# Optimization experiments

Hardware: AMD Instinct MI355X
Metric: run time of the kernel (lower is better)

The kernel has to match this reference:

```python
import jax, jax.numpy as jnp
import numpy as np
from jax import lax

N, D, H = 4096, 768, 16384


def setup_inputs() -> dict:
    key = jax.random.key(0)
    k0, k1, k2, k3, k4, k5, k6 = jax.random.split(key, 7)
    bound_e = 1.0 / np.sqrt(D)   # kaiming_uniform(a=sqrt(5)) on (H, D) -> bound 1/sqrt(fan_in)
    bound_d = 1.0 / np.sqrt(H)   # nn.Linear default init, fan_in = H
    return {
        "vision_embeddings": jax.random.normal(k0, (N, D), dtype=jnp.float32),
        "text_embeddings": jax.random.normal(k1, (N, D), dtype=jnp.float32),
        "encoder": jax.random.uniform(k2, (H, D), jnp.float32, -bound_e, bound_e),
        "Wv": jax.random.uniform(k3, (D, H), jnp.float32, -bound_d, bound_d),
        "bv": jax.random.uniform(k4, (D,), jnp.float32, -bound_d, bound_d),
        "Wt": jax.random.uniform(k5, (D, H), jnp.float32, -bound_d, bound_d),
        "bt": jax.random.uniform(k6, (D,), jnp.float32, -bound_d, bound_d),
        "topk": 32,
    }


def _l2norm(x, axis):
    return x / jnp.maximum(jnp.linalg.norm(x, axis=axis, keepdims=True), 1e-12)


def _encode(emb, encoder, topk):
    # F.normalize rows, then cdist(p=2) between unit vectors: ||a-b|| = sqrt(2-2 a.b)
    w = _l2norm(encoder, axis=1)            # [H, D]
    e = _l2norm(emb, axis=1)                # [N, D]
    cos = jnp.einsum("nd,hd->nh", e, w)     # [N, H]
    dist = jnp.sqrt(jnp.maximum(2.0 - 2.0 * cos, 0.0))
    sim = 2.0 - dist                         # [N, H]
    # kthvalue(abs, k=H-topk) == (topk+1)-th largest; keep strictly-greater entries
    abs_f = jnp.abs(sim)
    thres = lax.top_k(abs_f, topk + 1)[0][:, -1]  # [N]
    mask = (abs_f > thres[:, None]).astype(sim.dtype)
    return sim * mask


def reference(vision_embeddings, text_embeddings, encoder, Wv, bv, Wt, bt, topk):
    latent_v = _encode(vision_embeddings, encoder, topk)          # [N, H]
    recon_v = jnp.einsum("nh,dh->nd", latent_v, Wv) + bv          # [N, D]
    latent_t = _encode(text_embeddings, encoder, topk)            # [N, H]
    recon_t = jnp.einsum("nh,dh->nd", latent_t, Wt) + bt          # [N, D]
    return (recon_v, recon_t, latent_v, latent_t)
```

## Files before the change

### kernel.cpp

```cpp
#include <hip/hip_runtime.h>
#include <math.h>


#define N_ROWS 4096
#define D_DIM  768
#define H_DIM  16384
#define M_TOT  8192
#define TOPK   32
#define MARGIN 1e-3f
#define SEL_CAP 40
#define AMB_CAP 64
#define CAP2   512

typedef __attribute__((ext_vector_type(8))) short short8;
typedef __attribute__((ext_vector_type(4))) float floatx4;

__device__ inline unsigned short bf16_rne(float f) {
    unsigned u = __float_as_uint(f);
    unsigned r = u + 0x7fffu + ((u >> 16) & 1u);
    return (unsigned short)(r >> 16);
}

__device__ inline void gload16(const unsigned short* g, unsigned short* l) {
    __builtin_amdgcn_global_load_lds(
        (const __attribute__((address_space(1))) void*)g,
        (__attribute__((address_space(3))) void*)l, 16, 0, 0);
}

__global__ void split_all_kernel(const float* __restrict__ embv,
                                 const float* __restrict__ embt,
                                 const float* __restrict__ enc,
                                 unsigned short* __restrict__ Ahi,
                                 unsigned short* __restrict__ Alo,
                                 unsigned short* __restrict__ Bh,
                                 float* __restrict__ invA,
                                 float* __restrict__ invB)
{
    int row = blockIdx.x;
    int tid = threadIdx.x;
    const float* src;
    unsigned short *hi, *lo;
    float* invp;
    if (row < N_ROWS) {
        src = embv + (size_t)row * D_DIM;
        hi = Ahi + (size_t)row * D_DIM; lo = Alo + (size_t)row * D_DIM;
        invp = invA + row;
    } else if (row < 2 * N_ROWS) {
        int r = row - N_ROWS;
        src = embt + (size_t)r * D_DIM;
        hi = Ahi + (size_t)row * D_DIM; lo = Alo + (size_t)row * D_DIM;
        invp = invA + row;
    } else {
        int r = row - 2 * N_ROWS;
        src = enc + (size_t)r * D_DIM;
        hi = Bh + (size_t)r * D_DIM; lo = nullptr;
        invp = invB + r;
    }
    __shared__ float red[4];
    const float4* s4 = reinterpret_cast<const float4*>(src);
    float4 v = make_float4(0.f, 0.f, 0.f, 0.f);
    float ss = 0.f;
    if (tid < 192) {
        v = s4[tid];
        ss = v.x * v.x + v.y * v.y + v.z * v.z + v.w * v.w;
    }
    #pragma unroll
    for (int o = 32; o > 0; o >>= 1) ss += __shfl_down(ss, o);
    int wave = tid >> 6, lane = tid & 63;
    if (lane == 0) red[wave] = ss;
    __syncthreads();
    if (tid == 0) {
        float tot = red[0] + red[1] + red[2];
        red[0] = 1.f / fmaxf(sqrtf(tot), 1e-12f);
    }
    __syncthreads();
    float inv = red[0];
    if (tid == 0) *invp = inv;
    if (tid < 192) {
        float x[4] = {v.x * inv, v.y * inv, v.z * inv, v.w * inv};
        unsigned short hh[4], ll[4];
        #pragma unroll
        for (int t = 0; t < 4; t++) {
            hh[t] = bf16_rne(x[t]);
            float hf = __uint_as_float((unsigned)hh[t] << 16);
            ll[t] = bf16_rne(x[t] - hf);
        }
        ushort4 h4; h4.x = hh[0]; h4.y = hh[1]; h4.z = hh[2]; h4.w = hh[3];
        *reinterpret_cast<ushort4*>(hi + tid * 4) = h4;
        if (lo) {
            ushort4 l4; l4.x = ll[0]; l4.y = ll[1]; l4.z = ll[2]; l4.w = ll[3];
            *reinterpret_cast<ushort4*>(lo + tid * 4) = l4;
        }
    }
}

#define GBK 32

__global__ __launch_bounds__(256, 4)
void gemm_mfma_kernel(const unsigned short* __restrict__ Ahi,
                      const unsigned short* __restrict__ Alo,
                      const unsigned short* __restrict__ Bh,
                      float* __restrict__ latent)
{
    __shared__ unsigned short sA[2][128 * GBK];
    __shared__ unsigned short sB[128 * GBK];

    int tid = threadIdx.x;
    int lane = tid & 63;
    int wave = tid >> 6;
    int wr = (wave >> 1) * 64;
    int wc = (wave & 1) * 64;
    int m = lane & 15;
    int q = lane >> 4;

    int row0 = blockIdx.y * 128;
    int col0 = blockIdx.x * 128;

    int p0 = tid, p1 = tid + 256;
    int r0 = ((p0 >> 5) << 3) | (p0 & 7), q0 = (p0 >> 3) & 3;
    int r1 = ((p1 >> 5) << 3) | (p1 & 7), q1 = (p1 >> 3) & 3;
    size_t aoff0 = (size_t)(row0 + r0) * D_DIM + q0 * 8;
    size_t aoff1 = (size_t)(row0 + r1) * D_DIM + q1 * 8;
    size_t boff0 = (size_t)(col0 + r0) * D_DIM + q0 * 8;
    size_t boff1 = (size_t)(col0 + r1) * D_DIM + q1 * 8;

    int am0 = wr + m;
    int bn0 = wc + m;
    int offA = ((am0 >> 3) << 8) + (q << 6) + ((am0 & 7) << 3);
    int offB = ((bn0 >> 3) << 8) + (q << 6) + ((bn0 & 7) << 3);

    floatx4 acc[4][4];
    #pragma unroll
    for (int i = 0; i < 4; i++)
        #pragma unroll
        for (int j = 0; j < 4; j++)
            acc[i][j] = (floatx4){0.f, 0.f, 0.f, 0.f};

    for (int k0 = 0; k0 < D_DIM; k0 += GBK) {
        gload16(Ahi + aoff0 + k0, &sA[0][p0 * 8]);
        gload16(Ahi + aoff1 + k0, &sA[0][p1 * 8]);
        gload16(Alo + aoff0 + k0, &sA[1][p0 * 8]);
        gload16(Alo + aoff1 + k0, &sA[1][p1 * 8]);
        gload16(Bh + boff0 + k0, &sB[p0 * 8]);
        gload16(Bh + boff1 + k0, &sB[p1 * 8]);
        __syncthreads();

        short8 fah[4], fal[4];
        #pragma unroll
        for (int i = 0; i < 4; i++) {
            fah[i] = *(const short8*)&sA[0][offA + i * 512];
            fal[i] = *(const short8*)&sA[1][offA + i * 512];
        }
        #pragma unroll
        for (int j = 0; j < 4; j++) {
            short8 fb = *(const short8*)&sB[offB + j * 512];
            #pragma unroll
            for (int i = 0; i < 4; i++) {
                acc[i][j] = __builtin_amdgcn_mfma_f32_16x16x32_bf16(fah[i], fb, acc[i][j], 0, 0, 0);
                acc[i][j] = __builtin_amdgcn_mfma_f32_16x16x32_bf16(fal[i], fb, acc[i][j], 0, 0, 0);
            }
        }
        __syncthreads();
    }

    #pragma unroll
    for (int i = 0; i < 4; i++) {
        #pragma unroll
        for (int r = 0; r < 4; r++) {
            int grow = row0 + wr + i * 16 + q * 4 + r;
            float* dst = latent + (size_t)grow * H_DIM + col0 + wc + m;
            #pragma unroll
            for (int j = 0; j < 4; j++) {
                float cosv = acc[i][j][r];
                float sim = 2.f - sqrtf(fmaxf(2.f - 2.f * cosv, 0.f));
                dst[j * 16] = sim;
            }
        }
    }
}

__global__ __launch_bounds__(256)
void select_kernel(float* __restrict__ latent,
                   int* __restrict__ sel_cnt,
                   int* __restrict__ sel_idx,
                   float* __restrict__ sel_val,
                   int* __restrict__ amb_cnt,
                   int* __restrict__ amb_idx)
{
    int row = blockIdx.x;
    int tid = threadIdx.x;
    float* v = latent + (size_t)row * H_DIM;
    const float4* v4 = (const float4*)v;
    float4* vw = (float4*)v;

    __shared__ _Float16 hbuf[H_DIM];
    __shared__ float smax[256];
    __shared__ float sca[CAP2];
    __shared__ int   sci[CAP2];
    __shared__ float sT;
    __shared__ int scnt, svstar, skept, samb;

    float mx = -1.f;
    #pragma unroll 4
    for (int k = 0; k < 16; k++) {
        int i = tid + 256 * k;
        float4 x = v4[i];
        float a0 = fabsf(x.x), a1 = fabsf(x.y), a2 = fabsf(x.z), a3 = fabsf(x.w);
        hbuf[4 * i + 0] = (_Float16)a0;
        hbuf[4 * i + 1] = (_Float16)a1;
        hbuf[4 * i + 2] = (_Float16)a2;
        hbuf[4 * i + 3] = (_Float16)a3;
        mx = fmaxf(mx, fmaxf(fmaxf(a0, a1), fmaxf(a2, a3)));
    }
    smax[tid] = mx;
    if (tid == 0) { scnt = 0; svstar = 0x7FFFFFFF; skept = 0; samb = 0; }
    __syncthreads();

    int gt = 0;
    for (int j = 0; j < 256; j++) {
        float mj = smax[j];
        gt += (mj > mx || (mj == mx && j < tid)) ? 1 : 0;
    }
    if (gt == 32) sT = mx;
    __syncthreads();
    float Tm = sT - MARGIN;

    #pragma unroll 4
    for (int k = 0; k < 16; k++) {
        int i = tid + 256 * k;
        float a[4];
        a[0] = (float)hbuf[4 * i + 0]; a[1] = (float)hbuf[4 * i + 1];
        a[2] = (float)hbuf[4 * i + 2]; a[3] = (float)hbuf[4 * i + 3];
        bool any = (a[0] >= Tm) | (a[1] >= Tm) | (a[2] >= Tm) | (a[3] >= Tm);
        if (any) {
            #pragma unroll
            for (int t = 0; t < 4; t++) {
                if (a[t] >= Tm) {
                    int c = atomicAdd(&scnt, 1);
                    if (c < CAP2) { sci[c] = 4 * i + t; sca[c] = v[4 * i + t]; }
                }
            }
        }
        vw[i] = make_float4(0.f, 0.f, 0.f, 0.f);
    }
    __syncthreads();

    int C = min(scnt, CAP2);
    for (int c = tid; c < C; c += 256) {
        float a = fabsf(sca[c]);
        int g = 0;
        for (int j = 0; j < C; j++) {
            float aj = fabsf(sca[j]);
            g += (aj > a || (aj == a && j < c)) ? 1 : 0;
        }
        if (g <= TOPK) atomicMin(&svstar, __float_as_int(a));
    }
    __syncthreads();
    float vs = __int_as_float(svstar);

    for (int c = tid; c < C; c += 256) {
        float f = sca[c];
        float a = fabsf(f);
        int idx = sci[c];
        if (a > vs + MARGIN) {
            int s = atomicAdd(&skept, 1);
            sel_idx[(size_t)row * SEL_CAP + s] = idx;
            sel_val[(size_t)row * SEL_CAP + s] = f;
            v[idx] = f;
        } else if (a >= vs - MARGIN) {
            int s = atomicAdd(&samb, 1);
            if (s < AMB_CAP) amb_idx[(size_t)row * AMB_CAP + s] = idx;
        }
    }
    __syncthreads();
    if (tid == 0) { sel_cnt[row] = skept; amb_cnt[row] = min(samb, AMB_CAP); }
}

__global__ void refine_kernel(const float* __restrict__ embv,
                              const float* __restrict__ embt,
                              const float* __restrict__ enc,
                              const float* __restrict__ invA,
                              const float* __restrict__ invB,
                              float* __restrict__ latent,
                              int* __restrict__ sel_cnt,
                              int* __restrict__ sel_idx,
                              float* __restrict__ sel_val,
                              const int* __restrict__ amb_cnt,
                              const int* __restrict__ amb_idx)
{
    int row = blockIdx.x;
    int s = amb_cnt[row];
    if (s == 0) return;
    int tid = threadIdx.x;
    int m = sel_cnt[row];
    int need = TOPK - m;
    float* v = latent + (size_t)row * H_DIM;
    if (need <= 0) return;
    __shared__ float ex[AMB_CAP];
    __shared__ int evs, kc;
    const float* src = (row < N_ROWS) ? embv + (size_t)row * D_DIM
                                      : embt + (size_t)(row - N_ROWS) * D_DIM;
    float ia = invA[row];
    int wave = tid >> 6, lane = tid & 63;
    for (int a = wave; a < s; a += 4) {
        int h = amb_idx[(size_t)row * AMB_CAP + a];
        const float* w = enc + (size_t)h * D_DIM;
        float d = 0.f;
        for (int t = lane; t < D_DIM; t += 64) d += src[t] * w[t];
        #pragma unroll
        for (int o = 32; o > 0; o >>= 1) d += __shfl_down(d, o);
        if (lane == 0) {
            float cosv = d * ia * invB[h];
            ex[a] = 2.f - sqrtf(fmaxf(2.f - 2.f * cosv, 0.f));
        }
    }
    if (tid == 0) { evs = 0x7FFFFFFF; kc = 0; }
    __syncthreads();
    if (tid < s) {
        float mya = fabsf(ex[tid]);
        int g = 0;
        for (int j = 0; j < s; j++) {
            float aj = fabsf(ex[j]);
            g += (aj > mya || (aj == mya && j < tid)) ? 1 : 0;
        }
        if (g <= need) atomicMin(&evs, __float_as_int(mya));
    }
    __syncthreads();
    float ep = __int_as_float(evs);
    if (tid < s) {
        int idx = amb_idx[(size_t)row * AMB_CAP + tid];
        float e = ex[tid];
        if (fabsf(e) > ep) {
            int sl = atomicAdd(&kc, 1);
            v[idx] = e;
            sel_idx[(size_t)row * SEL_CAP + m + sl] = idx;
            sel_val[(size_t)row * SEL_CAP + m + sl] = e;
        }
    }
    __syncthreads();
    if (tid == 0) sel_cnt[row] = m + kc;
}

__global__ void transpose_kernel(const float* __restrict__ Wv,
                                 const float* __restrict__ Wt,
                                 float* __restrict__ WvT,
                                 float* __restrict__ WtT)
{
    int z = blockIdx.z;
    const float* W = z ? Wt : Wv;
    float* WT = z ? WtT : WvT;
    __shared__ float tile[32][33];
    int tx = threadIdx.x & 31;
    int ty = threadIdx.x >> 5;
    int h0 = blockIdx.x * 32;
    int d0 = blockIdx.y * 32;
    #pragma unroll
    for (int t = 0; t < 4; t++)
        tile[ty + t * 8][tx] = W[(size_t)(d0 + ty + t * 8) * H_DIM + h0 + tx];
    __syncthreads();
    #pragma unroll
    for (int t = 0; t < 4; t++)
        WT[(size_t)(h0 + ty + t * 8) * D_DIM + d0 + tx] = tile[tx][ty + t * 8];
}

__global__ void recon_kernel(const float* __restrict__ Wv_,
                             const float* __restrict__ Wt_,
                             const float* __restrict__ bv,
                             const float* __restrict__ bt,
                             const int* __restrict__ sel_cnt,
                             const int* __restrict__ sel_idx,
                             const float* __restrict__ sel_val,
                             long sh, long sd,
                             float* __restrict__ out)
{
    int n = blockIdx.x;
    int z = blockIdx.y;
    int row = z * N_ROWS + n;
    const float* W = z ? Wt_ : Wv_;
    const float* bias = z ? bt : bv;
    float* o = out + (size_t)z * N_ROWS * D_DIM + (size_t)n * D_DIM;

    __shared__ int s_idx[SEL_CAP];
    __shared__ float s_val[SEL_CAP];
    __shared__ int s_cnt;
    int tid = threadIdx.x;
    if (tid == 0) s_cnt = sel_cnt[row];
    __syncthreads();
    int cnt = s_cnt;
    if (tid < cnt) {
        s_idx[tid] = sel_idx[(size_t)row * SEL_CAP + tid];
        s_val[tid] = sel_val[(size_t)row * SEL_CAP + tid];
    }
    __syncthreads();

    for (int d = tid; d < D_DIM; d += 256) {
        float acc = bias[d];
        for (int j = 0; j < cnt; j++)
            acc += s_val[j] * W[(size_t)s_idx[j] * sh + (size_t)d * sd];
        o[d] = acc;
    }
}

__global__ void row_invnorm_kernel(const float* __restrict__ x,
                                   float* __restrict__ inv, int rows) {
    int row = blockIdx.x * 4 + (threadIdx.x >> 6);
    int lane = threadIdx.x & 63;
    if (row >= rows) return;
    const float4* p = reinterpret_cast<const float4*>(x + (size_t)row * D_DIM);
    float ss = 0.f;
    #pragma unroll
    for (int i = 0; i < 3; i++) {
        float4 v = p[lane + i * 64];
        ss += v.x * v.x + v.y * v.y + v.z * v.z + v.w * v.w;
    }
    #pragma unroll
    for (int off = 32; off > 0; off >>= 1) ss += __shfl_down(ss, off);
    if (lane == 0) inv[row] = 1.f / fmaxf(sqrtf(ss), 1e-12f);
}

#define BM 128
#define BN 128
#define BK 16
__global__ __launch_bounds__(256)
void gemm_sim_kernel(const float* __restrict__ embv,
                     const float* __restrict__ embt,
                     const float* __restrict__ enc,
                     const float* __restrict__ inv_emb,
                     const float* __restrict__ inv_enc,
                     float* __restrict__ latent)
{
    int z = blockIdx.z;
    const float* A = z ? embt : embv;
    const float* invA = inv_emb + z * N_ROWS;
    float* C = latent + (size_t)z * N_ROWS * H_DIM;
    __shared__ float As[BK][BM + 4];
    __shared__ float Bs[BK][BN + 4];
    int tid = threadIdx.x;
    int tx = tid & 15, ty = tid >> 4;
    int row0 = blockIdx.y * BM, col0 = blockIdx.x * BN;
    float acc[8][8];
    #pragma unroll
    for (int i = 0; i < 8; i++)
        #pragma unroll
        for (int j = 0; j < 8; j++) acc[i][j] = 0.f;
    for (int k0 = 0; k0 < D_DIM; k0 += BK) {
        #pragma unroll
        for (int t = 0; t < 2; t++) {
            int idx = t * 256 + tid;
            int r = idx >> 2, c4 = idx & 3;
            float4 va = *reinterpret_cast<const float4*>(
                A + (size_t)(row0 + r) * D_DIM + k0 + c4 * 4);
            As[c4 * 4 + 0][r] = va.x; As[c4 * 4 + 1][r] = va.y;
            As[c4 * 4 + 2][r] = va.z; As[c4 * 4 + 3][r] = va.w;
            float4 vb = *reinterpret_cast<const float4*>(
                enc + (size_t)(col0 + r) * D_DIM + k0 + c4 * 4);
            Bs[c4 * 4 + 0][r] = vb.x; Bs[c4 * 4 + 1][r] = vb.y;
            Bs[c4 * 4 + 2][r] = vb.z; Bs[c4 * 4 + 3][r] = vb.w;
        }
        __syncthreads();
        #pragma unroll
        for (int kk = 0; kk < BK; kk++) {
            float a[8], b[8];
            *reinterpret_cast<float4*>(&a[0]) = *reinterpret_cast<const float4*>(&As[kk][ty * 8]);
            *reinterpret_cast<float4*>(&a[4]) = *reinterpret_cast<const float4*>(&As[kk][ty * 8 + 4]);
            *reinterpret_cast<float4*>(&b[0]) = *reinterpret_cast<const float4*>(&Bs[kk][tx * 8]);
            *reinterpret_cast<float4*>(&b[4]) = *reinterpret_cast<const float4*>(&Bs[kk][tx * 8 + 4]);
            #pragma unroll
            for (int i = 0; i < 8; i++)
                #pragma unroll
                for (int j = 0; j < 8; j++)
                    acc[i][j] = fmaf(a[i], b[j], acc[i][j]);
        }
        __syncthreads();
    }
    #pragma unroll
    for (int i = 0; i < 8; i++) {
        int n = row0 + ty * 8 + i;
        float sa = invA[n];
        float* Crow = C + (size_t)n * H_DIM + col0 + tx * 8;
        float tmp[8];
        #pragma unroll
        for (int j = 0; j < 8; j++) {
            float cosv = acc[i][j] * sa * inv_enc[col0 + tx * 8 + j];
            tmp[j] = 2.f - sqrtf(fmaxf(2.f - 2.f * cosv, 0.f));
        }
        float4 o0 = {tmp[0], tmp[1], tmp[2], tmp[3]};
        float4 o1 = {tmp[4], tmp[5], tmp[6], tmp[7]};
        *reinterpret_cast<float4*>(Crow) = o0;
        *reinterpret_cast<float4*>(Crow + 4) = o1;
    }
}

__global__ void legacy_select_kernel(float* __restrict__ latent,
                                     const int* __restrict__ topk_p,
                                     int* __restrict__ sel_cnt,
                                     int* __restrict__ sel_idx,
                                     float* __restrict__ sel_val)
{
    int row = blockIdx.x;
    float* v = latent + (size_t)row * H_DIM;
    int tid = threadIdx.x;
    __shared__ unsigned hist[256];
    __shared__ unsigned s_prefix;
    __shared__ int s_k;
    __shared__ int s_cnt;
    int k = topk_p[0] + 1;
    unsigned prefix = 0;
    for (int shift = 24; shift >= 0; shift -= 8) {
        hist[tid] = 0;
        __syncthreads();
        unsigned pmask = (shift == 24) ? 0u : (0xFFFFFFFFu << (shift + 8));
        for (int i = tid; i < H_DIM; i += 256) {
            unsigned u = __float_as_uint(v[i]) & 0x7FFFFFFFu;
            if ((u & pmask) == prefix)
                atomicAdd(&hist[(u >> shift) & 255u], 1u);
        }
        __syncthreads();
        if (tid == 0) {
            int c = 0, b = 255;
            for (; b >= 0; b--) {
                c += (int)hist[b];
                if (c >= k) break;
            }
            if (b < 0) b = 0;
            s_prefix = prefix | ((unsigned)b << shift);
            s_k = k - (c - (int)hist[b]);
        }
        __syncthreads();
        prefix = s_prefix;
        k = s_k;
        __syncthreads();
    }
    float thres = __uint_as_float(prefix);
    if (tid == 0) s_cnt = 0;
    __syncthreads();
    for (int i = tid; i < H_DIM; i += 256) {
        float x = v[i];
        bool keep = (fabsf(x) > thres);
        v[i] = keep ? x : 0.f;
        if (keep) {
            int slot = atomicAdd(&s_cnt, 1);
            if (slot < SEL_CAP) {
                sel_idx[(size_t)row * SEL_CAP + slot] = i;
                sel_val[(size_t)row * SEL_CAP + slot] = x;
            }
        }
    }
    __syncthreads();
    if (tid == 0) sel_cnt[row] = (s_cnt > SEL_CAP) ? SEL_CAP : s_cnt;
}

extern "C" void kernel_launch(void* const* d_in, const int* in_sizes, int n_in,
                              void* d_out, int out_size, void* d_ws, size_t ws_size,
                              hipStream_t stream) {
    const float* embv = (const float*)d_in[0];
    const float* embt = (const float*)d_in[1];
    const float* enc  = (const float*)d_in[2];
    const float* Wv   = (const float*)d_in[3];
    const float* bv   = (const float*)d_in[4];
    const float* Wt   = (const float*)d_in[5];
    const float* bt   = (const float*)d_in[6];
    const int* topk   = (const int*)d_in[7];
    float* out = (float*)d_out;

    float* recon_out = out;
    float* latent = out + (size_t)2 * N_ROWS * D_DIM;

    char* ws = (char*)d_ws;
    size_t off = 0;
    float* invA = (float*)(ws + off);            off += (size_t)M_TOT * 4;
    float* invB = (float*)(ws + off);            off += (size_t)H_DIM * 4;
    int*   sel_cnt = (int*)(ws + off);           off += (size_t)M_TOT * 4;
    int*   amb_cnt = (int*)(ws + off);           off += (size_t)M_TOT * 4;
    int*   sel_idx = (int*)(ws + off);           off += (size_t)M_TOT * SEL_CAP * 4;
    float* sel_val = (float*)(ws + off);         off += (size_t)M_TOT * SEL_CAP * 4;
    int*   amb_idx = (int*)(ws + off);           off += (size_t)M_TOT * AMB_CAP * 4;
    unsigned short* Ahi = (unsigned short*)(ws + off); off += (size_t)M_TOT * D_DIM * 2;
    unsigned short* Alo = (unsigned short*)(ws + off); off += (size_t)M_TOT * D_DIM * 2;
    unsigned short* Bh  = (unsigned short*)(ws + off); off += (size_t)H_DIM * D_DIM * 2;
    size_t core_need = off;
    float* WvT = (float*)(ws + off);
    float* WtT = WvT + (size_t)D_DIM * H_DIM;
    size_t full_need = off + (size_t)2 * D_DIM * H_DIM * 4;

    if (ws_size >= core_need) {
        bool use_T = ws_size >= full_need;

        split_all_kernel<<<2 * N_ROWS + H_DIM, 256, 0, stream>>>(
            embv, embt, enc, Ahi, Alo, Bh, invA, invB);

        gemm_mfma_kernel<<<dim3(H_DIM / 128, M_TOT / 128), 256, 0, stream>>>(
            Ahi, Alo, Bh, latent);

        select_kernel<<<M_TOT, 256, 0, stream>>>(latent,
            sel_cnt, sel_idx, sel_val, amb_cnt, amb_idx);

        refine_kernel<<<M_TOT, 256, 0, stream>>>(embv, embt, enc, invA, invB,
            latent, sel_cnt, sel_idx, sel_val, amb_cnt, amb_idx);

        if (use_T) {
            transpose_kernel<<<dim3(H_DIM / 32, D_DIM / 32, 2), 256, 0, stream>>>(
                Wv, Wt, WvT, WtT);
            recon_kernel<<<dim3(N_ROWS, 2), 256, 0, stream>>>(
                WvT, WtT, bv, bt, sel_cnt, sel_idx, sel_val, (long)D_DIM, 1L, recon_out);
        } else {
            recon_kernel<<<dim3(N_ROWS, 2), 256, 0, stream>>>(
                Wv, Wt, bv, bt, sel_cnt, sel_idx, sel_val, 1L, (long)H_DIM, recon_out);
        }
    } else {
        size_t o2 = 0;
        float* inv_enc = (float*)(ws + o2); o2 += (size_t)H_DIM * 4;
        float* inv_emb = (float*)(ws + o2); o2 += (size_t)2 * N_ROWS * 4;
        int*   l_cnt = (int*)(ws + o2);     o2 += (size_t)2 * N_ROWS * 4;
        int*   l_idx = (int*)(ws + o2);     o2 += (size_t)2 * N_ROWS * SEL_CAP * 4;
        float* l_val = (float*)(ws + o2);   o2 += (size_t)2 * N_ROWS * SEL_CAP * 4;
        row_invnorm_kernel<<<H_DIM / 4, 256, 0, stream>>>(enc, inv_enc, H_DIM);
        row_invnorm_kernel<<<N_ROWS / 4, 256, 0, stream>>>(embv, inv_emb, N_ROWS);
        row_invnorm_kernel<<<N_ROWS / 4, 256, 0, stream>>>(embt, inv_emb + N_ROWS, N_ROWS);
        dim3 g(H_DIM / BN, N_ROWS / BM, 2);
        gemm_sim_kernel<<<g, 256, 0, stream>>>(embv, embt, enc, inv_emb, inv_enc, latent);
        legacy_select_kernel<<<2 * N_ROWS, 256, 0, stream>>>(latent, topk, l_cnt, l_idx, l_val);
        recon_kernel<<<dim3(N_ROWS, 2), 256, 0, stream>>>(
            Wv, Wt, bv, bt, l_cnt, l_idx, l_val, 1L, (long)H_DIM, recon_out);
    }
}
```

Baseline: 1.716 ms.

## Write similarity matrix as fp16 to workspace and select from registers

The GEMM epilogue now writes the similarity values as fp16 into a separate workspace buffer instead of fp32 into the latent output. This halves the GEMM store traffic and lets the select kernel read half as many bytes, keeping them in registers rather than an LDS staging buffer. The latent rows are then zero-filled with plain writes, and the candidate and ambiguity margins become relative to the threshold to absorb fp16 rounding, with refine expected to recompute exact values for ambiguous entries. Launch bounds occupancy is raised, and the old fp32 path is kept as a fallback for smaller workspaces. The risks are extra workspace memory and fp16 precision near the top-k boundary.

New measurement: 4.538 ms. 2.64x slower.

```diff
diff --git a/kernel.cpp b/kernel.cpp
--- a/kernel.cpp
+++ b/kernel.cpp
@@ -7,7 +7,6 @@
 #define H_DIM  16384
 #define M_TOT  8192
 #define TOPK   32
-#define MARGIN 1e-3f
 #define SEL_CAP 40
 #define AMB_CAP 64
 #define CAP2   512
@@ -96,11 +95,11 @@
 
 #define GBK 32
 
-__global__ __launch_bounds__(256, 4)
+__global__ __launch_bounds__(256, 6)
 void gemm_mfma_kernel(const unsigned short* __restrict__ Ahi,
                       const unsigned short* __restrict__ Alo,
                       const unsigned short* __restrict__ Bh,
-                      float* __restrict__ latent)
+                      _Float16* __restrict__ simh)
 {
     __shared__ unsigned short sA[2][128 * GBK];
     __shared__ unsigned short sB[128 * GBK];
@@ -168,19 +167,20 @@
         #pragma unroll
         for (int r = 0; r < 4; r++) {
             int grow = row0 + wr + i * 16 + q * 4 + r;
-            float* dst = latent + (size_t)grow * H_DIM + col0 + wc + m;
+            _Float16* dst = simh + (size_t)grow * H_DIM + col0 + wc + m;
             #pragma unroll
             for (int j = 0; j < 4; j++) {
                 float cosv = acc[i][j][r];
                 float sim = 2.f - sqrtf(fmaxf(2.f - 2.f * cosv, 0.f));
-                dst[j * 16] = sim;
+                dst[j * 16] = (_Float16)sim;
             }
         }
     }
 }
 
 __global__ __launch_bounds__(256)
-void select_kernel(float* __restrict__ latent,
+void select_kernel(const _Float16* __restrict__ simh,
+                   float* __restrict__ latent,
                    int* __restrict__ sel_cnt,
                    int* __restrict__ sel_idx,
                    float* __restrict__ sel_val,
@@ -189,28 +189,24 @@
 {
     int row = blockIdx.x;
     int tid = threadIdx.x;
+    const uint4* s4 = (const uint4*)(simh + (size_t)row * H_DIM);
+    float4* vw = (float4*)(latent + (size_t)row * H_DIM);
     float* v = latent + (size_t)row * H_DIM;
-    const float4* v4 = (const float4*)v;
-    float4* vw = (float4*)v;
-
-    __shared__ _Float16 hbuf[H_DIM];
+
     __shared__ float smax[256];
     __shared__ float sca[CAP2];
     __shared__ int   sci[CAP2];
     __shared__ float sT;
     __shared__ int scnt, svstar, skept, samb;
 
+    uint4 regs[8];
     float mx = -1.f;
-    #pragma unroll 4
-    for (int k = 0; k < 16; k++) {
-        int i = tid + 256 * k;
-        float4 x = v4[i];
-        float a0 = fabsf(x.x), a1 = fabsf(x.y), a2 = fabsf(x.z), a3 = fabsf(x.w);
-        hbuf[4 * i + 0] = (_Float16)a0;
-        hbuf[4 * i + 1] = (_Float16)a1;
-        hbuf[4 * i + 2] = (_Float16)a2;
-        hbuf[4 * i + 3] = (_Float16)a3;
-        mx = fmaxf(mx, fmaxf(fmaxf(a0, a1), fmaxf(a2, a3)));
+    #pragma unroll
+    for (int k = 0; k < 8; k++) {
+        regs[k] = s4[tid + 256 * k];
+        const _Float16* h = (const _Float16*)&regs[k];
+        #pragma unroll
+        for (int t = 0; t < 8; t++) mx = fmaxf(mx, fabsf((float)h[t]));
     }
     smax[tid] = mx;
     if (tid == 0) { scnt = 0; svstar = 0x7FFFFFFF; skept = 0; samb = 0; }
@@ -223,26 +219,25 @@
     }
     if (gt == 32) sT = mx;
     __syncthreads();
-    float Tm = sT - MARGIN;
-
-    #pragma unroll 4
-    for (int k = 0; k < 16; k++) {
-        int i = tid + 256 * k;
-        float a[4];
-        a[0] = (float)hbuf[4 * i + 0]; a[1] = (float)hbuf[4 * i + 1];
-        a[2] = (float)hbuf[4 * i + 2]; a[3] = (float)hbuf[4 * i + 3];
-        bool any = (a[0] >= Tm) | (a[1] >= Tm) | (a[2] >= Tm) | (a[3] >= Tm);
-        if (any) {
-            #pragma unroll
-            for (int t = 0; t < 4; t++) {
-                if (a[t] >= Tm) {
-                    int c = atomicAdd(&scnt, 1);
-                    if (c < CAP2) { sci[c] = 4 * i + t; sca[c] = v[4 * i + t]; }
-                }
+    float T = sT;
+    float Tm = T - (T * 1.953125e-3f + 6e-4f);
+
+    #pragma unroll
+    for (int k = 0; k < 8; k++) {
+        const _Float16* h = (const _Float16*)&regs[k];
+        int base = (tid + 256 * k) * 8;
+        #pragma unroll
+        for (int t = 0; t < 8; t++) {
+            float f = (float)h[t];
+            if (fabsf(f) >= Tm) {
+                int c = atomicAdd(&scnt, 1);
+                if (c < CAP2) { sci[c] = base + t; sca[c] = f; }
             }
         }
-        vw[i] = make_float4(0.f, 0.f, 0.f, 0.f);
-    }
+    }
+    float4 z = make_float4(0.f, 0.f, 0.f, 0.f);
+    #pragma unroll
+    for (int k = 0; k < 16; k++) vw[tid + 256 * k] = z;
     __syncthreads();
 
     int C = min(scnt, CAP2);
@@ -257,17 +252,18 @@
     }
     __syncthreads();
     float vs = __int_as_float(svstar);
+    float M = vs * 9.765625e-4f + 3e-4f;
 
     for (int c = tid; c < C; c += 256) {
         float f = sca[c];
         float a = fabsf(f);
         int idx = sci[c];
-        if (a > vs + MARGIN) {
+        if (a > vs + M) {
             int s = atomicAdd(&skept, 1);
             sel_idx[(size_t)row * SEL_CAP + s] = idx;
             sel_val[(size_t)row * SEL_CAP + s] = f;
             v[idx] = f;
-        } else if (a >= vs - MARGIN) {
+        } else if (a >= vs - M) {
             int s = atomicAdd(&samb, 1);
             if (s < AMB_CAP) amb_idx[(size_t)row * AMB_CAP + s] = idx;
         }
@@ -401,6 +397,162 @@
     }
 }
 
+__global__ __launch_bounds__(256, 6)
+void gemm_mfma_f32_kernel(const unsigned short* __restrict__ Ahi,
+                          const unsigned short* __restrict__ Alo,
+                          const unsigned short* __restrict__ Bh,
+                          float* __restrict__ latent)
+{
+    __shared__ unsigned short sA[2][128 * GBK];
+    __shared__ unsigned short sB[128 * GBK];
+    int tid = threadIdx.x;
+    int lane = tid & 63, wave = tid >> 6;
+    int wr = (wave >> 1) * 64, wc = (wave & 1) * 64;
+    int m = lane & 15, q = lane >> 4;
+    int row0 = blockIdx.y * 128, col0 = blockIdx.x * 128;
+    int p0 = tid, p1 = tid + 256;
+    int r0 = ((p0 >> 5) << 3) | (p0 & 7), q0 = (p0 >> 3) & 3;
+    int r1 = ((p1 >> 5) << 3) | (p1 & 7), q1 = (p1 >> 3) & 3;
+    size_t aoff0 = (size_t)(row0 + r0) * D_DIM + q0 * 8;
+    size_t aoff1 = (size_t)(row0 + r1) * D_DIM + q1 * 8;
+    size_t boff0 = (size_t)(col0 + r0) * D_DIM + q0 * 8;
+    size_t boff1 = (size_t)(col0 + r1) * D_DIM + q1 * 8;
+    int am0 = wr + m, bn0 = wc + m;
+    int offA = ((am0 >> 3) << 8) + (q << 6) + ((am0 & 7) << 3);
+    int offB = ((bn0 >> 3) << 8) + (q << 6) + ((bn0 & 7) << 3);
+    floatx4 acc[4][4];
+    #pragma unroll
+    for (int i = 0; i < 4; i++)
+        #pragma unroll
+        for (int j = 0; j < 4; j++) acc[i][j] = (floatx4){0.f, 0.f, 0.f, 0.f};
+    for (int k0 = 0; k0 < D_DIM; k0 += GBK) {
+        gload16(Ahi + aoff0 + k0, &sA[0][p0 * 8]);
+        gload16(Ahi + aoff1 + k0, &sA[0][p1 * 8]);
+        gload16(Alo + aoff0 + k0, &sA[1][p0 * 8]);
+        gload16(Alo + aoff1 + k0, &sA[1][p1 * 8]);
+        gload16(Bh + boff0 + k0, &sB[p0 * 8]);
+        gload16(Bh + boff1 + k0, &sB[p1 * 8]);
+        __syncthreads();
+        short8 fah[4], fal[4];
+        #pragma unroll
+        for (int i = 0; i < 4; i++) {
+            fah[i] = *(const short8*)&sA[0][offA + i * 512];
+            fal[i] = *(const short8*)&sA[1][offA + i * 512];
+        }
+        #pragma unroll
+        for (int j = 0; j < 4; j++) {
+            short8 fb = *(const short8*)&sB[offB + j * 512];
+            #pragma unroll
+            for (int i = 0; i < 4; i++) {
+                acc[i][j] = __builtin_amdgcn_mfma_f32_16x16x32_bf16(fah[i], fb, acc[i][j], 0, 0, 0);
+                acc[i][j] = __builtin_amdgcn_mfma_f32_16x16x32_bf16(fal[i], fb, acc[i][j], 0, 0, 0);
+            }
+        }
+        __syncthreads();
+    }
+    #pragma unroll
+    for (int i = 0; i < 4; i++) {
+        #pragma unroll
+        for (int r = 0; r < 4; r++) {
+            int grow = row0 + wr + i * 16 + q * 4 + r;
+            float* dst = latent + (size_t)grow * H_DIM + col0 + wc + m;
+            #pragma unroll
+            for (int j = 0; j < 4; j++) {
+                float cosv = acc[i][j][r];
+                dst[j * 16] = 2.f - sqrtf(fmaxf(2.f - 2.f * cosv, 0.f));
+            }
+        }
+    }
+}
+
+__global__ __launch_bounds__(256)
+void select_f32_kernel(float* __restrict__ latent,
+                       int* __restrict__ sel_cnt,
+                       int* __restrict__ sel_idx,
+                       float* __restrict__ sel_val,
+                       int* __restrict__ amb_cnt,
+                       int* __restrict__ amb_idx)
+{
+    int row = blockIdx.x;
+    int tid = threadIdx.x;
+    float* v = latent + (size_t)row * H_DIM;
+    const float4* v4 = (const float4*)v;
+    float4* vw = (float4*)v;
+    __shared__ _Float16 hbuf[H_DIM];
+    __shared__ float smax[256];
+    __shared__ float sca[CAP2];
+    __shared__ int   sci[CAP2];
+    __shared__ float sT;
+    __shared__ int scnt, svstar, skept, samb;
+    float mx = -1.f;
+    #pragma unroll 4
+    for (int k = 0; k < 16; k++) {
+        int i = tid + 256 * k;
+        float4 x = v4[i];
+        float a0 = fabsf(x.x), a1 = fabsf(x.y), a2 = fabsf(x.z), a3 = fabsf(x.w);
+        hbuf[4 * i + 0] = (_Float16)a0; hbuf[4 * i + 1] = (_Float16)a1;
+        hbuf[4 * i + 2] = (_Float16)a2; hbuf[4 * i + 3] = (_Float16)a3;
+        mx = fmaxf(mx, fmaxf(fmaxf(a0, a1), fmaxf(a2, a3)));
+    }
+    smax[tid] = mx;
+    if (tid == 0) { scnt = 0; svstar = 0x7FFFFFFF; skept = 0; samb = 0; }
+    __syncthreads();
+    int gt = 0;
+    for (int j = 0; j < 256; j++) {
+        float mj = smax[j];
+        gt += (mj > mx || (mj == mx && j < tid)) ? 1 : 0;
+    }
+    if (gt == 32) sT = mx;
+    __syncthreads();
+    float Tm = sT - 1e-3f;
+    #pragma unroll 4
+    for (int k = 0; k < 16; k++) {
+        int i = tid + 256 * k;
+        float a[4];
+        a[0] = (float)hbuf[4 * i + 0]; a[1] = (float)hbuf[4 * i + 1];
+        a[2] = (float)hbuf[4 * i + 2]; a[3] = (float)hbuf[4 * i + 3];
+        if ((a[0] >= Tm) | (a[1] >= Tm) | (a[2] >= Tm) | (a[3] >= Tm)) {
+            #pragma unroll
+            for (int t = 0; t < 4; t++) {
+                if (a[t] >= Tm) {
+                    int c = atomicAdd(&scnt, 1);
+                    if (c < CAP2) { sci[c] = 4 * i + t; sca[c] = v[4 * i + t]; }
+                }
+            }
+        }
+        vw[i] = make_float4(0.f, 0.f, 0.f, 0.f);
+    }
+    __syncthreads();
+    int C = min(scnt, CAP2);
+    for (int c = tid; c < C; c += 256) {
+        float a = fabsf(sca[c]);
+        int g = 0;
+        for (int j = 0; j < C; j++) {
+            float aj = fabsf(sca[j]);
+            g += (aj > a || (aj == a && j < c)) ? 1 : 0;
+        }
+        if (g <= TOPK) atomicMin(&svstar, __float_as_int(a));
+    }
+    __syncthreads();
+    float vs = __int_as_float(svstar);
+    for (int c = tid; c < C; c += 256) {
+        float f = sca[c];
+        float a = fabsf(f);
+        int idx = sci[c];
+        if (a > vs + 1e-3f) {
+            int s = atomicAdd(&skept, 1);
+            sel_idx[(size_t)row * SEL_CAP + s] = idx;
+            sel_val[(size_t)row * SEL_CAP + s] = f;
+            v[idx] = f;
+        } else if (a >= vs - 1e-3f) {
+            int s = atomicAdd(&samb, 1);
+            if (s < AMB_CAP) amb_idx[(size_t)row * AMB_CAP + s] = idx;
+        }
+    }
+    __syncthreads();
+    if (tid == 0) { sel_cnt[row] = skept; amb_cnt[row] = min(samb, AMB_CAP); }
+}
+
 __global__ void row_invnorm_kernel(const float* __restrict__ x,
                                    float* __restrict__ inv, int rows) {
     int row = blockIdx.x * 4 + (threadIdx.x >> 6);
@@ -518,17 +670,13 @@
         __syncthreads();
         if (tid == 0) {
             int c = 0, b = 255;
-            for (; b >= 0; b--) {
-                c += (int)hist[b];
-                if (c >= k) break;
-            }
+            for (; b >= 0; b--) { c += (int)hist[b]; if (c >= k) break; }
             if (b < 0) b = 0;
             s_prefix = prefix | ((unsigned)b << shift);
             s_k = k - (c - (int)hist[b]);
         }
         __syncthreads();
-        prefix = s_prefix;
-        k = s_k;
+        prefix = s_prefix; k = s_k;
         __syncthreads();
     }
     float thres = __uint_as_float(prefix);
@@ -578,31 +726,51 @@
     unsigned short* Ahi = (unsigned short*)(ws + off); off += (size_t)M_TOT * D_DIM * 2;
     unsigned short* Alo = (unsigned short*)(ws + off); off += (size_t)M_TOT * D_DIM * 2;
     unsigned short* Bh  = (unsigned short*)(ws + off); off += (size_t)H_DIM * D_DIM * 2;
-    size_t core_need = off;
-    float* WvT = (float*)(ws + off);
+    size_t base_need = off;
+
+    _Float16* simh = (_Float16*)(ws + off);
+    size_t sim_need = off + (size_t)M_TOT * H_DIM * 2;
+    float* WvT = (float*)(ws + sim_need);
     float* WtT = WvT + (size_t)D_DIM * H_DIM;
-    size_t full_need = off + (size_t)2 * D_DIM * H_DIM * 4;
-
-    if (ws_size >= core_need) {
+    size_t full_need = sim_need + (size_t)2 * D_DIM * H_DIM * 4;
+    float* WvT_c = (float*)(ws + base_need);
+    float* WtT_c = WvT_c + (size_t)D_DIM * H_DIM;
+    size_t tierc_full = base_need + (size_t)2 * D_DIM * H_DIM * 4;
+
+    if (ws_size >= sim_need) {
         bool use_T = ws_size >= full_need;
-
         split_all_kernel<<<2 * N_ROWS + H_DIM, 256, 0, stream>>>(
             embv, embt, enc, Ahi, Alo, Bh, invA, invB);
-
         gemm_mfma_kernel<<<dim3(H_DIM / 128, M_TOT / 128), 256, 0, stream>>>(
-            Ahi, Alo, Bh, latent);
-
-        select_kernel<<<M_TOT, 256, 0, stream>>>(latent,
+            Ahi, Alo, Bh, simh);
+        select_kernel<<<M_TOT, 256, 0, stream>>>(simh, latent,
             sel_cnt, sel_idx, sel_val, amb_cnt, amb_idx);
-
         refine_kernel<<<M_TOT, 256, 0, stream>>>(embv, embt, enc, invA, invB,
             latent, sel_cnt, sel_idx, sel_val, amb_cnt, amb_idx);
-
         if (use_T) {
             transpose_kernel<<<dim3(H_DIM / 32, D_DIM / 32, 2), 256, 0, stream>>>(
                 Wv, Wt, WvT, WtT);
             recon_kernel<<<dim3(N_ROWS, 2), 256, 0, stream>>>(
                 WvT, WtT, bv, bt, sel_cnt, sel_idx, sel_val, (long)D_DIM, 1L, recon_out);
+        } else {
+            recon_kernel<<<dim3(N_ROWS, 2), 256, 0, stream>>>(
+                Wv, Wt, bv, bt, sel_cnt, sel_idx, sel_val, 1L, (long)H_DIM, recon_out);
+        }
+    } else if (ws_size >= base_need) {
+        bool use_T = ws_size >= tierc_full;
+        split_all_kernel<<<2 * N_ROWS + H_DIM, 256, 0, stream>>>(
+            embv, embt, enc, Ahi, Alo, Bh, invA, invB);
+        gemm_mfma_f32_kernel<<<dim3(H_DIM / 128, M_TOT / 128), 256, 0, stream>>>(
+            Ahi, Alo, Bh, latent);
+        select_f32_kernel<<<M_TOT, 256, 0, stream>>>(latent,
+            sel_cnt, sel_idx, sel_val, amb_cnt, amb_idx);
+        refine_kernel<<<M_TOT, 256, 0, stream>>>(embv, embt, enc, invA, invB,
+            latent, sel_cnt, sel_idx, sel_val, amb_cnt, amb_idx);
+        if (use_T) {
+            transpose_kernel<<<dim3(H_DIM / 32, D_DIM / 32, 2), 256, 0, stream>>>(
+                Wv, Wt, WvT_c, WtT_c);
+            recon_kernel<<<dim3(N_ROWS, 2), 256, 0, stream>>>(
+                WvT_c, WtT_c, bv, bt, sel_cnt, sel_idx, sel_val, (long)D_DIM, 1L, recon_out);
         } else {
             recon_kernel<<<dim3(N_ROWS, 2), 256, 0, stream>>>(
                 Wv, Wt, bv, bt, sel_cnt, sel_idx, sel_val, 1L, (long)H_DIM, recon_out);
```
